# Performance work log

Hardware: AMD Instinct MI355X
Metric: run time of the kernel (lower is better)

Reference implementation:

```python
import jax, jax.numpy as jnp
import numpy as np

N_QUBITS = 4
Q_DEPTH = 6
Q_DELTA = 0.01


def _conv1d(x, w, b):
    # x: (B, Cin, L), w: (Cout, Cin, 3), padding=1
    y = jax.lax.conv_general_dilated(x, w, window_strides=(1,), padding=[(1, 1)],
                                     dimension_numbers=('NCH', 'OIH', 'NCH'))
    return y + b[None, :, None]


def _maxpool2(x):
    B, C, L = x.shape
    return x.reshape(B, C, L // 2, 2).max(axis=-1)


def _take(state, i, axis):
    return jax.lax.index_in_dim(state, i, axis, keepdims=False)


def _apply_ry(state, theta, wire):
    # state: (B, 2, 2, 2, 2); theta: scalar (shared weight) or (B,) (per-sample)
    half = theta * 0.5
    c, s = jnp.cos(half), jnp.sin(half)
    if c.ndim == 1:  # per-sample angles -> broadcast over remaining qubit axes
        c = c.reshape(-1, 1, 1, 1)
        s = s.reshape(-1, 1, 1, 1)
    ax = wire + 1
    s0 = _take(state, 0, ax)
    s1 = _take(state, 1, ax)
    return jnp.stack([c * s0 - s * s1, s * s0 + c * s1], axis=ax)


def _apply_cnot(state, ctrl, tgt):
    cax, tax = ctrl + 1, tgt + 1
    a0 = jax.lax.slice_in_dim(state, 0, 1, axis=cax)
    a1 = jax.lax.slice_in_dim(state, 1, 2, axis=cax)
    return jnp.concatenate([a0, jnp.flip(a1, axis=tax)], axis=cax)


def _quantum_forward(q_in, q_params):
    # Batched 4-qubit state-vector simulation (PennyLane default.qubit semantics,
    # wire 0 = most significant -> axis wire+1 of (B,2,2,2,2) state).
    B = q_in.shape[0]
    # H layer on |0000> -> uniform amplitude 1/4
    state = jnp.full((B, 2, 2, 2, 2), 0.25, dtype=q_in.dtype)
    for w in range(N_QUBITS):
        state = _apply_ry(state, q_in[:, w], w)
    qw = q_params.reshape(Q_DEPTH, N_QUBITS)
    for k in range(Q_DEPTH):
        # entangling layer: CNOT(0,1), CNOT(2,3), then CNOT(1,2)
        state = _apply_cnot(state, 0, 1)
        state = _apply_cnot(state, 2, 3)
        state = _apply_cnot(state, 1, 2)
        for w in range(N_QUBITS):
            state = _apply_ry(state, qw[k, w], w)
    probs = state * state  # real amplitudes throughout (H as initial |+>^n, RY, CNOT)
    zs = [(_take(probs, 0, q + 1) - _take(probs, 1, q + 1)).sum(axis=(1, 2, 3))
          for q in range(N_QUBITS)]
    return jnp.stack(zs, axis=1)  # (B, 4) <Z_q>


def setup_inputs() -> dict:
    key = jax.random.key(0)
    ks = jax.random.split(key, 12)
    B, F = 32768, 64
    FLAT = 64 * (F // 4)  # 1024
    return {
        'x': jax.random.normal(ks[0], (B, F), jnp.float32),
        'conv1_w': jax.random.normal(ks[1], (32, 1, 3), jnp.float32) * 0.3,
        'conv1_b': jax.random.normal(ks[2], (32,), jnp.float32) * 0.05,
        'conv2_w': jax.random.normal(ks[3], (64, 32, 3), jnp.float32) * 0.05,
        'conv2_b': jax.random.normal(ks[4], (64,), jnp.float32) * 0.05,
        'fc_w': jax.random.normal(ks[5], (FLAT, 64), jnp.float32) * (1.0 / np.sqrt(FLAT)),
        'fc_b': jax.random.normal(ks[6], (64,), jnp.float32) * 0.05,
        'pre_w': jax.random.normal(ks[7], (64, N_QUBITS), jnp.float32) * 0.125,
        'pre_b': jax.random.normal(ks[8], (N_QUBITS,), jnp.float32) * 0.05,
        'q_params': Q_DELTA * jax.random.normal(ks[9], (Q_DEPTH * N_QUBITS,), jnp.float32),
        'post_w': jax.random.normal(ks[10], (N_QUBITS, 1), jnp.float32) * 0.5,
        'post_b': jax.random.normal(ks[11], (1,), jnp.float32) * 0.05,
    }


def reference(x, conv1_w, conv1_b, conv2_w, conv2_b, fc_w, fc_b,
              pre_w, pre_b, q_params, post_w, post_b):
    h = x[:, None, :]  # (B, 1, F)
    h = _maxpool2(jax.nn.relu(_conv1d(h, conv1_w, conv1_b)))   # (B, 32, F/2)
    h = _maxpool2(jax.nn.relu(_conv1d(h, conv2_w, conv2_b)))   # (B, 64, F/4)
    h = h.reshape(h.shape[0], -1)                              # (B, 1024)
    h = jax.nn.relu(h @ fc_w + fc_b)                           # (B, 64)
    q_in = jnp.tanh(h @ pre_w + pre_b) * (np.pi / 2.0)         # (B, 4)
    q_out = _quantum_forward(q_in, q_params)                   # (B, 4)
    return jax.nn.sigmoid(q_out @ post_w + post_b)             # (B, 1)
```

## Files before the change

kernel.cpp:

```cpp
#include <hip/hip_runtime.h>
#include <math.h>

typedef unsigned short u16;
typedef unsigned int u32;
typedef __attribute__((ext_vector_type(8))) short bf16x8;
typedef __attribute__((ext_vector_type(4))) float f32x4;
typedef __attribute__((ext_vector_type(2))) float f32x2;

__device__ __forceinline__ u16 f32_to_bf16(float f) {
    u32 u = __float_as_uint(f);
    u32 r = u + 0x7FFFu + ((u >> 16) & 1u);
    return (u16)(r >> 16);
}
__device__ __forceinline__ u32 pack2(u16 a, u16 b) { return (u32)a | ((u32)b << 16); }

__device__ __forceinline__ u32 rne_bits(float f) {
    u32 u = __float_as_uint(f);
    return u + 0x7FFFu + ((u >> 16) & 1u);
}
__device__ __forceinline__ u32 pack_rne(float a, float b) {
    return __builtin_amdgcn_perm(rne_bits(b), rne_bits(a), 0x07060302u);
}

__device__ __forceinline__ float fast_tanh(float x) {
    float e = __expf(2.f * x);
    return 1.f - 2.f / (e + 1.f);
}

template<int STRIDE>
__device__ __forceinline__ void ry_gate(float st[16], float theta) {
    float s, c;
    sincosf(theta * 0.5f, &s, &c);
#pragma unroll
    for (int i = 0; i < 16; ++i) {
        if (i & STRIDE) continue;
        float s0 = st[i], s1 = st[i | STRIDE];
        st[i]          = c * s0 - s * s1;
        st[i | STRIDE] = fmaf(s, s0, c * s1);
    }
}
template<int CS, int TS>
__device__ __forceinline__ void cnot_gate(float st[16]) {
#pragma unroll
    for (int i = 0; i < 16; ++i) {
        if ((i & CS) && !(i & TS)) {
            float tmp = st[i]; st[i] = st[i | TS]; st[i | TS] = tmp;
        }
    }
}

__global__ __launch_bounds__(256) void prep_kernel(
    const float* __restrict__ fcw, const float* __restrict__ w2,
    const float* __restrict__ qp,
    u16* __restrict__ whi, u16* __restrict__ w2b, float* __restrict__ Mg)
{
    const int f  = blockIdx.x;
    const int k0 = threadIdx.x * 4;
    u16 hv[4];
#pragma unroll
    for (int i = 0; i < 4; ++i) {
        int k  = k0 + i;
        int op = k >> 6, oc = k & 63;
        hv[i] = f32_to_bf16(fcw[(size_t)(oc * 16 + op) * 64 + f]);
    }
    *(uint2*)(whi + (size_t)f * 1024 + k0) = make_uint2(pack2(hv[0], hv[1]), pack2(hv[2], hv[3]));

    if (threadIdx.x < 96) {
        const int j  = threadIdx.x;
        const int ic = j / 3, t = j - ic * 3;
        w2b[(t * 64 + f) * 32 + ic] = f32_to_bf16(w2[f * 96 + j]);
    }

    if (blockIdx.x == 0 && threadIdx.x < 16) {
        const int j = threadIdx.x;
        float st[16];
#pragma unroll
        for (int i = 0; i < 16; ++i) st[i] = (i == j) ? 1.f : 0.f;
        for (int k = 0; k < 6; ++k) {
            cnot_gate<8, 4>(st);
            cnot_gate<2, 1>(st);
            cnot_gate<4, 2>(st);
            ry_gate<8>(st, qp[k * 4 + 0]);
            ry_gate<4>(st, qp[k * 4 + 1]);
            ry_gate<2>(st, qp[k * 4 + 2]);
            ry_gate<1>(st, qp[k * 4 + 3]);
        }
#pragma unroll
        for (int i = 0; i < 16; ++i) Mg[i * 16 + j] = st[i];
    }
}

__global__ __launch_bounds__(512, 4) void fused_kernel(
    const float* __restrict__ x,
    const float* __restrict__ w1, const float* __restrict__ b1,
    const u16* __restrict__ w2b, const float* __restrict__ b2,
    const u16* __restrict__ whi,
    const float* __restrict__ fcb,
    const float* __restrict__ prew, const float* __restrict__ preb,
    const float* __restrict__ postw, const float* __restrict__ postb,
    const float* __restrict__ Mg,
    float* __restrict__ out)
{
    __shared__ __align__(16) u16 c1h[16 * 1384];
    __shared__ __align__(16) float part2[2 * 1280];
    __shared__ float prews[256];
    __shared__ float Ms[16][17];
    __shared__ float fcbs[64];

    const int tid  = threadIdx.x;
    const int bs   = blockIdx.x * 16;
    const int wv   = tid >> 6, lane = tid & 63;
    const int lr   = lane & 15, lq = lane >> 4;

    if (tid < 256) {
        prews[tid] = prew[tid];
        Ms[tid >> 4][tid & 15] = Mg[tid];
    }
    if (tid < 64) fcbs[tid] = fcb[tid];

    const int s1 = tid >> 5;
    const int pp = tid & 31;
    const float* xb = x + (size_t)(bs + s1) * 64;
    const int j = 2 * pp;
    float xm1 = (j == 0)  ? 0.f : xb[j - 1];
    float x0  = xb[j];
    float x1  = xb[j + 1];
    float xp2 = (j == 62) ? 0.f : xb[j + 2];

    bf16x8 af[3][4];
#pragma unroll
    for (int t = 0; t < 3; ++t)
#pragma unroll
        for (int mt = 0; mt < 4; ++mt)
            af[t][mt] = *(const bf16x8*)(w2b + (size_t)(t * 64 + mt * 16 + lr) * 32 + lq * 8);
    f32x4 bias2[4];
#pragma unroll
    for (int mt = 0; mt < 4; ++mt)
        bias2[mt] = *(const f32x4*)(b2 + mt * 16 + lq * 4);

    {
        u16* sbase = c1h + s1 * 1384;
        if (pp == 0 || pp == 31) {
            uint4 z = make_uint4(0, 0, 0, 0);
            uint4* zr = (uint4*)(sbase + (pp == 0 ? 0 : 33) * 40);
            zr[0] = z; zr[1] = z; zr[2] = z; zr[3] = z;
        }
        const f32x2 A1 = {xm1, x0};
        const f32x2 A2 = {x0,  x1};
        const f32x2 A3 = {x1,  xp2};
        u32 row[16];
#pragma unroll
        for (int icp = 0; icp < 16; ++icp) {
            float v[2];
#pragma unroll
            for (int h2 = 0; h2 < 2; ++h2) {
                int ic = icp * 2 + h2;
                float wa = w1[ic * 3], wb = w1[ic * 3 + 1], wc = w1[ic * 3 + 2], bb = b1[ic];
                f32x2 Y = {bb, bb};
                Y += wa * A1;
                Y += wb * A2;
                Y += wc * A3;
                v[h2] = fmaxf(fmaxf(Y.x, Y.y), 0.f);
            }
            row[icp] = pack_rne(v[0], v[1]);
        }
        uint4* d = (uint4*)(sbase + (1 + pp) * 40);
        d[0] = make_uint4(row[0],  row[1],  row[2],  row[3]);
        d[1] = make_uint4(row[4],  row[5],  row[6],  row[7]);
        d[2] = make_uint4(row[8],  row[9],  row[10], row[11]);
        d[3] = make_uint4(row[12], row[13], row[14], row[15]);
    }

#pragma unroll
    for (int nt = 0; nt < 4; ++nt) {
        const int s  = wv * 2 + (nt >> 1);
        const int qb = (nt & 1) * 16;
        const u16* bp = c1h + s * 1384 + (qb + lr) * 40 + lq * 8;
        bf16x8 bf0 = *(const bf16x8*)(bp);
        bf16x8 bf1 = *(const bf16x8*)(bp + 40);
        bf16x8 bf2 = *(const bf16x8*)(bp + 80);
        const int op = (qb + lr) >> 1;
#pragma unroll
        for (int mt = 0; mt < 4; ++mt) {
            f32x4 acc = __builtin_amdgcn_mfma_f32_16x16x32_bf16(af[0][mt], bf0, bias2[mt], 0, 0, 0);
            acc = __builtin_amdgcn_mfma_f32_16x16x32_bf16(af[1][mt], bf1, acc, 0, 0, 0);
            acc = __builtin_amdgcn_mfma_f32_16x16x32_bf16(af[2][mt], bf2, acc, 0, 0, 0);
            float p0 = fmaxf(fmaxf(acc[0], __shfl_xor(acc[0], 1)), 0.f);
            float p1 = fmaxf(fmaxf(acc[1], __shfl_xor(acc[1], 1)), 0.f);
            float p2 = fmaxf(fmaxf(acc[2], __shfl_xor(acc[2], 1)), 0.f);
            float p3 = fmaxf(fmaxf(acc[3], __shfl_xor(acc[3], 1)), 0.f);
            if (!(lane & 1)) {
                *(uint2*)(c1h + s * 1384 + op * 72 + mt * 16 + lq * 4) =
                    make_uint2(pack_rne(p0, p1), pack_rne(p2, p3));
            }
        }
    }
    __syncthreads();

    const int g  = wv & 3;
    const int hf = wv >> 2;
    const int n0 = g * 16;
    f32x4 acc0 = {0.f, 0.f, 0.f, 0.f};
    {
        const u16* ab0 = c1h + (size_t)lr * 1384 + lq * 8;
        const u16* bh0 = whi + (size_t)(n0 + lr) * 1024 + hf * 16 * 32 + lq * 8;
#pragma unroll
        for (int i = 0; i < 16; ++i) {
            const int kc = hf * 16 + i;
            const int aoff = (kc >> 1) * 72 + (kc & 1) * 32;
            bf16x8 a0 = *(const bf16x8*)(ab0 + aoff);
            bf16x8 f0 = *(const bf16x8*)(bh0 + i * 32);
            acc0 = __builtin_amdgcn_mfma_f32_16x16x32_bf16(a0, f0, acc0, 0, 0, 0);
        }
    }
    *(f32x4*)(&part2[hf * 1280 + (n0 + lr) * 20 + lq * 4]) = acc0;
    __syncthreads();

    if (wv == 0) {
        const int L = lane & 3;
        const int s = lane >> 2;

        float a0 = 0.f, a1 = 0.f, a2 = 0.f, a3 = 0.f;
#pragma unroll
        for (int i2 = 0; i2 < 4; ++i2) {
#pragma unroll
            for (int c = 0; c < 4; ++c) {
                int ff = L * 16 + i2 * 4 + c;
                float hx = fmaxf(part2[ff * 20 + s] + part2[1280 + ff * 20 + s] + fcbs[ff], 0.f);
                float4 pw = *(const float4*)&prews[ff * 4];
                a0 = fmaf(hx, pw.x, a0);
                a1 = fmaf(hx, pw.y, a1);
                a2 = fmaf(hx, pw.z, a2);
                a3 = fmaf(hx, pw.w, a3);
            }
        }
        a0 += __shfl_xor(a0, 1); a0 += __shfl_xor(a0, 2);
        a1 += __shfl_xor(a1, 1); a1 += __shfl_xor(a1, 2);
        a2 += __shfl_xor(a2, 1); a2 += __shfl_xor(a2, 2);
        a3 += __shfl_xor(a3, 1); a3 += __shfl_xor(a3, 2);

        const float HP = 1.5707963267948966f;
        float qin[4] = { fast_tanh(a0 + preb[0]) * HP, fast_tanh(a1 + preb[1]) * HP,
                         fast_tanh(a2 + preb[2]) * HP, fast_tanh(a3 + preb[3]) * HP };

        float va[4], vb[4];
        const float RS = 0.70710678118654752f;
#pragma unroll
        for (int w = 0; w < 4; ++w) {
            float sw, cw;
            __sincosf(qin[w] * 0.5f, &sw, &cw);
            va[w] = (cw - sw) * RS;
            vb[w] = (sw + cw) * RS;
        }
        float sv[16];
#pragma unroll
        for (int jj = 0; jj < 16; ++jj) {
            float t = (jj & 8) ? vb[0] : va[0];
            t *= (jj & 4) ? vb[1] : va[1];
            t *= (jj & 2) ? vb[2] : va[2];
            t *= (jj & 1) ? vb[3] : va[3];
            sv[jj] = t;
        }
        float z0 = 0.f, z1 = 0.f, z2 = 0.f, z3 = 0.f;
#pragma unroll
        for (int rr = 0; rr < 4; ++rr) {
            const int r = L * 4 + rr;
            float m = 0.f;
#pragma unroll
            for (int jj = 0; jj < 16; ++jj) m = fmaf(Ms[r][jj], sv[jj], m);
            float p = m * m;
            z0 += (r & 8) ? -p : p;
            z1 += (r & 4) ? -p : p;
            z2 += (r & 2) ? -p : p;
            z3 += (r & 1) ? -p : p;
        }
        z0 += __shfl_xor(z0, 1); z0 += __shfl_xor(z0, 2);
        z1 += __shfl_xor(z1, 1); z1 += __shfl_xor(z1, 2);
        z2 += __shfl_xor(z2, 1); z2 += __shfl_xor(z2, 2);
        z3 += __shfl_xor(z3, 1); z3 += __shfl_xor(z3, 2);

        if (L == 0) {
            float t = postb[0] + z0 * postw[0] + z1 * postw[1] + z2 * postw[2] + z3 * postw[3];
            out[bs + s] = 1.f / (1.f + __expf(-t));
        }
    }
}

extern "C" void kernel_launch(void* const* d_in, const int* in_sizes, int n_in,
                              void* d_out, int out_size, void* d_ws, size_t ws_size,
                              hipStream_t stream) {
    const float* x     = (const float*)d_in[0];
    const float* w1    = (const float*)d_in[1];
    const float* b1    = (const float*)d_in[2];
    const float* w2    = (const float*)d_in[3];
    const float* b2    = (const float*)d_in[4];
    const float* fcw   = (const float*)d_in[5];
    const float* fcb   = (const float*)d_in[6];
    const float* prew  = (const float*)d_in[7];
    const float* preb  = (const float*)d_in[8];
    const float* qp    = (const float*)d_in[9];
    const float* postw = (const float*)d_in[10];
    const float* postb = (const float*)d_in[11];
    float* out = (float*)d_out;

    u16*   fwhi = (u16*)d_ws;
    float* Mg   = (float*)((char*)d_ws + 131072);
    u16*   w2b  = (u16*)((char*)d_ws + 132096);

    const int B = in_sizes[0] / 64;

    prep_kernel<<<dim3(64), dim3(256), 0, stream>>>(fcw, w2, qp, fwhi, w2b, Mg);
    fused_kernel<<<dim3(B / 16), dim3(512), 0, stream>>>(x, w1, b1, w2b, b2,
                                                         fwhi, fcb, prew, preb,
                                                         postw, postb, Mg, out);
}
```

Baseline: 135.7 us.

## Use hardware bf16 pack, shuffle conv halos, split FC accumulators, stagger LDS reads

Swaps the software round-to-nearest-even bf16 packing for the v_cvt_pk_bf16_f32 instruction. Replaces two of the four per-thread global loads of x with a single float2 load, getting the neighbouring halo values through lane shuffles. Splits the FC MFMA chain across two independent accumulators to shorten the dependency chain, and rotates the final reduction's index order per lane to reduce LDS bank conflicts. Each piece is a small micro-optimization in a short, latency-bound kernel, and the shuffle path relies on the 32 threads of a sample sitting contiguously inside one wavefront.

Measured after the change: 135.6 us. No clear change (-0.0%).

```diff
diff --git a/kernel.cpp b/kernel.cpp
--- a/kernel.cpp
+++ b/kernel.cpp
@@ -14,12 +14,10 @@
 }
 __device__ __forceinline__ u32 pack2(u16 a, u16 b) { return (u32)a | ((u32)b << 16); }
 
-__device__ __forceinline__ u32 rne_bits(float f) {
-    u32 u = __float_as_uint(f);
-    return u + 0x7FFFu + ((u >> 16) & 1u);
-}
-__device__ __forceinline__ u32 pack_rne(float a, float b) {
-    return __builtin_amdgcn_perm(rne_bits(b), rne_bits(a), 0x07060302u);
+__device__ __forceinline__ u32 cvt_pk_bf16(float a, float b) {
+    u32 r;
+    asm("v_cvt_pk_bf16_f32 %0, %1, %2" : "=v"(r) : "v"(a), "v"(b));
+    return r;
 }
 
 __device__ __forceinline__ float fast_tanh(float x) {
@@ -122,10 +120,8 @@
     const int pp = tid & 31;
     const float* xb = x + (size_t)(bs + s1) * 64;
     const int j = 2 * pp;
-    float xm1 = (j == 0)  ? 0.f : xb[j - 1];
-    float x0  = xb[j];
-    float x1  = xb[j + 1];
-    float xp2 = (j == 62) ? 0.f : xb[j + 2];
+    const float2 xv = *(const float2*)(xb + j);
+    float x0 = xv.x, x1 = xv.y;
 
     bf16x8 af[3][4];
 #pragma unroll
@@ -137,6 +133,9 @@
 #pragma unroll
     for (int mt = 0; mt < 4; ++mt)
         bias2[mt] = *(const f32x4*)(b2 + mt * 16 + lq * 4);
+
+    float xm1 = __shfl_up(x1, 1);   if (pp == 0)  xm1 = 0.f;
+    float xp2 = __shfl_down(x0, 1); if (pp == 31) xp2 = 0.f;
 
     {
         u16* sbase = c1h + s1 * 1384;
@@ -162,7 +161,7 @@
                 Y += wc * A3;
                 v[h2] = fmaxf(fmaxf(Y.x, Y.y), 0.f);
             }
-            row[icp] = pack_rne(v[0], v[1]);
+            row[icp] = cvt_pk_bf16(v[0], v[1]);
         }
         uint4* d = (uint4*)(sbase + (1 + pp) * 40);
         d[0] = make_uint4(row[0],  row[1],  row[2],  row[3]);
@@ -191,7 +190,7 @@
             float p3 = fmaxf(fmaxf(acc[3], __shfl_xor(acc[3], 1)), 0.f);
             if (!(lane & 1)) {
                 *(uint2*)(c1h + s * 1384 + op * 72 + mt * 16 + lq * 4) =
-                    make_uint2(pack_rne(p0, p1), pack_rne(p2, p3));
+                    make_uint2(cvt_pk_bf16(p0, p1), cvt_pk_bf16(p2, p3));
             }
         }
     }
@@ -200,19 +199,26 @@
     const int g  = wv & 3;
     const int hf = wv >> 2;
     const int n0 = g * 16;
-    f32x4 acc0 = {0.f, 0.f, 0.f, 0.f};
+    f32x4 accA = {0.f, 0.f, 0.f, 0.f};
+    f32x4 accB = {0.f, 0.f, 0.f, 0.f};
     {
         const u16* ab0 = c1h + (size_t)lr * 1384 + lq * 8;
         const u16* bh0 = whi + (size_t)(n0 + lr) * 1024 + hf * 16 * 32 + lq * 8;
 #pragma unroll
-        for (int i = 0; i < 16; ++i) {
-            const int kc = hf * 16 + i;
-            const int aoff = (kc >> 1) * 72 + (kc & 1) * 32;
-            bf16x8 a0 = *(const bf16x8*)(ab0 + aoff);
+        for (int i = 0; i < 16; i += 2) {
+            const int kcA = hf * 16 + i;
+            const int kcB = kcA + 1;
+            const int aoffA = (kcA >> 1) * 72 + (kcA & 1) * 32;
+            const int aoffB = (kcB >> 1) * 72 + (kcB & 1) * 32;
+            bf16x8 a0 = *(const bf16x8*)(ab0 + aoffA);
+            bf16x8 a1 = *(const bf16x8*)(ab0 + aoffB);
             bf16x8 f0 = *(const bf16x8*)(bh0 + i * 32);
-            acc0 = __builtin_amdgcn_mfma_f32_16x16x32_bf16(a0, f0, acc0, 0, 0, 0);
-        }
-    }
+            bf16x8 f1 = *(const bf16x8*)(bh0 + (i + 1) * 32);
+            accA = __builtin_amdgcn_mfma_f32_16x16x32_bf16(a0, f0, accA, 0, 0, 0);
+            accB = __builtin_amdgcn_mfma_f32_16x16x32_bf16(a1, f1, accB, 0, 0, 0);
+        }
+    }
+    const f32x4 acc0 = accA + accB;
     *(f32x4*)(&part2[hf * 1280 + (n0 + lr) * 20 + lq * 4]) = acc0;
     __syncthreads();
 
@@ -225,7 +231,8 @@
         for (int i2 = 0; i2 < 4; ++i2) {
 #pragma unroll
             for (int c = 0; c < 4; ++c) {
-                int ff = L * 16 + i2 * 4 + c;
+                int cc = (c + L) & 3;
+                int ff = L * 16 + i2 * 4 + cc;
                 float hx = fmaxf(part2[ff * 20 + s] + part2[1280 + ff * 20 + s] + fcbs[ff], 0.f);
                 float4 pw = *(const float4*)&prews[ff * 4];
                 a0 = fmaf(hx, pw.x, a0);
```
